# Kernel optimization log

Hardware: AMD Instinct MI355X
Metric: run time of the kernel (lower is better)

## Reference

```python
import jax, jax.numpy as jnp
import numpy as np
from jax import lax

STATE_SIZE = 80
HIDDEN = 512
NC = 1
H = W = 32
STEPS = 64  # steps_range=(64,64)
THRESH = 0.01


def _maxpool3(x):
    # MaxPool2d(3, stride=1, padding=1) on NCHW
    return lax.reduce_window(x, -jnp.inf, lax.max, (1, 1, 3, 3), (1, 1, 1, 1), 'SAME')


def _conv3x3(x, w, b):
    y = lax.conv_general_dilated(x, w, (1, 1), 'SAME',
                                 dimension_numbers=('NCHW', 'OIHW', 'NCHW'))
    return y + b[None, :, None, None]


def _conv1x1(x, w, b):
    # w: (O, I, 1, 1) -> pointwise einsum
    return jnp.einsum('oi,bihw->bohw', w[:, :, 0, 0], x) + b[None, :, None, None]


def setup_inputs() -> dict:
    key = jax.random.key(0)
    ks = jax.random.split(key, 7)
    z = jax.random.normal(ks[0], (8, 100, 1, 1), dtype=jnp.float32)
    W1 = jax.random.normal(ks[1], (HIDDEN, STATE_SIZE, 3, 3), jnp.float32) / np.sqrt(STATE_SIZE * 9)
    b1 = jax.random.normal(ks[2], (HIDDEN,), jnp.float32) * 0.01
    W2 = jax.random.normal(ks[3], (HIDDEN, HIDDEN, 1, 1), jnp.float32) / np.sqrt(HIDDEN)
    b2 = jax.random.normal(ks[4], (HIDDEN,), jnp.float32) * 0.01
    # original code zero-inits the last conv; use small random weights so grads flow
    W3 = jax.random.normal(ks[5], (STATE_SIZE, HIDDEN, 1, 1), jnp.float32) * (0.01 / np.sqrt(HIDDEN))
    b3 = jax.random.normal(ks[6], (STATE_SIZE,), jnp.float32) * 0.001
    return {'z': z, 'W1': W1, 'b1': b1, 'W2': W2, 'b2': b2, 'W3': W3, 'b3': b3}


def _forward(z, W1, b1, W2, b2, W3, b3):
    N = z.shape[0]
    cH, cW = H // 2, W // 2
    state = jnp.zeros((N, STATE_SIZE, H, W), dtype=z.dtype)
    init_hidden = z[:, :STATE_SIZE - 1, 0, 0]  # (N, 79)
    state = state.at[:, 1:, cH, cW].set(init_hidden)
    state = state.at[:, 0, cH, cW].set(1.0)

    keys = jax.random.split(jax.random.key(42), STEPS)

    def ca_step(state, step_key):
        pre_living = _maxpool3(state[:, 0:1]) > THRESH
        perception = _conv3x3(state, W1, b1)
        h = jax.nn.relu(_conv1x1(perception, W2, b2))
        updates = _conv1x1(h, W3, b3)
        # stochastic update with p=1 (rand < 1 is always True, kept for fidelity)
        mask = jax.random.uniform(step_key, (state.shape[0], 1, H, W)) < 1.0
        state = state + mask.astype(state.dtype) * updates
        post_living = _maxpool3(state[:, 0:1]) > THRESH
        living = (post_living & pre_living).astype(state.dtype)
        return state * living, None

    state, _ = lax.scan(ca_step, state, keys)
    return state[:, :NC]  # (N, 1, H, W)


def reference(z, W1, b1, W2, b2, W3, b3):
    return _forward(z, W1, b1, W2, b2, W3, b3)
```

## Files before the change

### kernel.cpp

```cpp
#include <hip/hip_runtime.h>


#define NPIX 8192
#define T_ALIVE 0.01f

typedef _Float16 f16;
typedef __attribute__((ext_vector_type(8)))  _Float16 h8_t;
typedef __attribute__((ext_vector_type(4)))  _Float16 h4_t;
typedef __attribute__((ext_vector_type(16))) float    fx16;

__global__ __launch_bounds__(256) void tr512(
    const float* __restrict__ W2, float* __restrict__ W2T)
{
    __shared__ float t[32][33];
    const int bx = blockIdx.x & 15, by = blockIdx.x >> 4;
    const int x = threadIdx.x & 31, y8 = threadIdx.x >> 5;
#pragma unroll
    for (int r = 0; r < 32; r += 8)
        t[r + y8][x] = W2[(size_t)(by * 32 + r + y8) * 512 + bx * 32 + x];
    __syncthreads();
#pragma unroll
    for (int r = 0; r < 32; r += 8)
        W2T[(size_t)(bx * 32 + r + y8) * 512 + by * 32 + x] = t[x][r + y8];
}

__global__ __launch_bounds__(256) void wc32(
    const float* __restrict__ W2T, const float* __restrict__ W1,
    float* __restrict__ Wc)
{
    __shared__ float As[16][32];
    __shared__ float Bs[16][32];
    const int tid = threadIdx.x;
    const int ty = tid >> 3, tx = tid & 7;
    const int m0 = blockIdx.y * 32, n0 = blockIdx.x * 32;
    float acc[4] = {0.f, 0.f, 0.f, 0.f};

    for (int k0 = 0; k0 < 512; k0 += 16) {
#pragma unroll
        for (int t = 0; t < 2; ++t) {
            const int idx = tid + t * 256;
            const int r = idx >> 5, c = idx & 31;
            As[r][c] = W2T[(size_t)(k0 + r) * 512 + m0 + c];
            const int n = n0 + c;
            Bs[r][c] = (n < 720) ? W1[(size_t)(k0 + r) * 720 + n] : 0.f;
        }
        __syncthreads();
#pragma unroll
        for (int kk = 0; kk < 16; ++kk) {
            const float a = As[kk][ty];
#pragma unroll
            for (int j = 0; j < 4; ++j)
                acc[j] = fmaf(a, Bs[kk][tx * 4 + j], acc[j]);
        }
        __syncthreads();
    }
    const int m = m0 + ty;
#pragma unroll
    for (int j = 0; j < 4; ++j) {
        const int n = n0 + tx * 4 + j;
        if (n < 720) Wc[(size_t)m * 720 + n] = acc[j];
    }
}

__global__ __launch_bounds__(256) void bc_k(
    const float* __restrict__ W2, const float* __restrict__ b1,
    const float* __restrict__ b2, float* __restrict__ bc)
{
    const int m = blockIdx.x * 256 + threadIdx.x;
    if (m >= 512) return;
    float a = b2[m];
    for (int h = 0; h < 512; ++h) a += W2[m * 512 + h] * b1[h];
    bc[m] = a;
}

__global__ __launch_bounds__(256) void swz_wc2(
    const float* __restrict__ Wc, f16* __restrict__ Wcsw2)
{
    const int idx = blockIdx.x * 256 + threadIdx.x;
    if (idx >= 45 * 16 * 64) return;
    const int lane = idx & 63;
    const int t = idx >> 6;
    const int mtg = t & 15, ks = t >> 4;
    const int m = mtg * 32 + (lane & 31);
    const int k0 = ks * 16 + (lane >> 5) * 8;
    h8_t v;
#pragma unroll
    for (int j = 0; j < 8; ++j) {
        const int kp = k0 + j;
        const int tap = kp / 80, ci = kp - tap * 80;
        v[j] = (f16)Wc[(size_t)m * 720 + ci * 9 + tap];
    }
    *(h8_t*)(Wcsw2 + (size_t)idx * 8) = v;
}

__global__ __launch_bounds__(256) void swz_w32(
    const float* __restrict__ W3, f16* __restrict__ W3sw2)
{
    const int idx = blockIdx.x * 256 + threadIdx.x;
    if (idx >= 32 * 3 * 64) return;
    const int lane = idx & 63;
    const int t = idx >> 6;
    const int mt = t % 3, ks2 = t / 3;
    const int m = mt * 32 + (lane & 31);
    const int k0 = ks2 * 16 + (lane >> 5) * 8;
    h8_t v;
#pragma unroll
    for (int j = 0; j < 8; ++j)
        v[j] = (f16)((m < 80) ? W3[(size_t)m * 512 + k0 + j] : 0.f);
    *(h8_t*)(W3sw2 + (size_t)idx * 8) = v;
}

__global__ __launch_bounds__(256) void seed2(
    const float* __restrict__ z, float* __restrict__ U0,
    float* __restrict__ A0)
{
    const int idx = blockIdx.x * 256 + threadIdx.x;
    if (idx >= 640) return;
    const int b = idx / 80, c = idx - b * 80;
    const int n = b * 1024 + 16 * 32 + 16;
    const float v = (c == 0) ? 1.f : z[b * 100 + (c - 1)];
    U0[(size_t)c * NPIX + n] = v;
    if (c == 0) A0[n] = 1.f;
}

__global__ __launch_bounds__(512) void kS(
    const f16* __restrict__ Wcsw2, const float* __restrict__ bc,
    const f16* __restrict__ W3sw2, const float* __restrict__ b3,
    const float* __restrict__ Uin, const float* __restrict__ Ain,
    float* __restrict__ Uout, float* __restrict__ Aout)
{
    __shared__ f16   msT[8160];
    __shared__ f16   Hsw[16384];
    __shared__ float bcL[512];
    __shared__ float b3L[80];
    __shared__ float SrowL[2560];
    __shared__ float N5[160];
    __shared__ float A5[160];
    __shared__ float live3[96];

    const int tid = threadIdx.x;
    const int lane = tid & 63, w = tid >> 6;
    const int li = lane & 31, q2 = lane >> 5;
    const int blk = blockIdx.x;
    const int b = blk >> 5, y = blk & 31;
    const int gb = b * 1024;

    h8_t abuf[8][2];
#pragma unroll
    for (int pk = 0; pk < 8; ++pk)
#pragma unroll
        for (int i = 0; i < 2; ++i)
            abuf[pk][i] = *(const h8_t*)(Wcsw2 +
                (((size_t)pk * 16 + (w * 2 + i)) * 64 + lane) * 8);

    bcL[tid] = bc[tid];
    if (tid < 80) b3L[tid] = b3[tid];

    if (tid < 160) {
        const int r = tid >> 5, x = tid & 31, yy = y - 2 + r;
        const bool ok = ((unsigned)yy < 32u);
        N5[tid] = ok ? Uin[gb + yy * 32 + x] : -1e30f;
        A5[tid] = ok ? Ain[gb + yy * 32 + x] : -1e30f;
    }
    {
        h8_t zz;
#pragma unroll
        for (int j = 0; j < 8; ++j) zz[j] = (f16)0.f;
        for (int i = tid; i < 1020; i += 512)
            *(h8_t*)(msT + (size_t)i * 8) = zz;
    }
    __syncthreads();

    if (tid < 96) {
        const int r = tid >> 5, x = tid & 31;
        float mN = -1e30f, mA = -1e30f;
#pragma unroll
        for (int rr = 0; rr < 3; ++rr)
#pragma unroll
            for (int dx = -1; dx <= 1; ++dx) {
                const int xx = x + dx;
                if ((unsigned)xx < 32u) {
                    mN = fmaxf(mN, N5[(r + rr) * 32 + xx]);
                    mA = fmaxf(mA, A5[(r + rr) * 32 + xx]);
                }
            }
        live3[tid] = (mN > T_ALIVE && mA > T_ALIVE) ? 1.f : 0.f;
    }
    __syncthreads();

#pragma unroll
    for (int it = 0; it < 15; ++it) {
        const int e = tid + it * 512;
        const int x = e & 31;
        const int t2 = e >> 5;
        const int r = t2 / 80, ch = t2 - r * 80;
        const int yy = y - 1 + r;
        float v = 0.f;
        if ((unsigned)yy < 32u)
            v = Uin[(size_t)ch * NPIX + gb + yy * 32 + x] * live3[r * 32 + x];
        msT[(size_t)((ch >> 3) * 102 + r * 34 + x + 1) * 8 + (ch & 7)] = (f16)v;
        if (r == 1) {
            SrowL[ch * 32 + x] = v;
            if (ch == 0) Aout[gb + y * 32 + x] = v;
        }
    }
    __syncthreads();

    int pxh[9];
#pragma unroll
    for (int t = 0; t < 9; ++t)
        pxh[t] = ((t / 3) * 34 + li + (t % 3)) * 8;

    fx16 acc[2];
#pragma unroll
    for (int i = 0; i < 2; ++i)
#pragma unroll
        for (int r = 0; r < 16; ++r) acc[i][r] = 0.f;

#pragma unroll
    for (int ks = 0; ks < 45; ++ks) {
        const int o0 = 2 * ks, o1 = 2 * ks + 1;
        const int a0 = (o0 % 10) * 816 + pxh[o0 / 10];
        const int a1 = (o1 % 10) * 816 + pxh[o1 / 10];
        const h8_t bf = *(const h8_t*)(msT + (q2 ? a1 : a0));
        h8_t av[2];
#pragma unroll
        for (int i = 0; i < 2; ++i) av[i] = abuf[ks & 7][i];
        if (ks + 8 < 45) {
#pragma unroll
            for (int i = 0; i < 2; ++i)
                abuf[ks & 7][i] = *(const h8_t*)(Wcsw2 +
                    (((size_t)(ks + 8) * 16 + (w * 2 + i)) * 64 + lane) * 8);
        }
#pragma unroll
        for (int i = 0; i < 2; ++i)
            acc[i] = __builtin_amdgcn_mfma_f32_32x32x16_f16(
                av[i], bf, acc[i], 0, 0, 0);
    }

#pragma unroll
    for (int i = 0; i < 2; ++i) {
#pragma unroll
        for (int aa = 0; aa < 4; ++aa) {
            const int chl = i * 32 + 8 * aa + 4 * q2;
            const int co = w * 8 + i * 4 + aa;
            h4_t v4;
#pragma unroll
            for (int rb = 0; rb < 4; ++rb)
                v4[rb] = (f16)fmaxf(acc[i][aa * 4 + rb] + bcL[w * 64 + chl + rb], 0.f);
            *(h4_t*)(Hsw + ((size_t)co * 32 + li) * 8 + 4 * q2) = v4;
        }
    }
    __syncthreads();

    if (w < 3) {
        const int mt = w;
        h8_t ar[8];
#pragma unroll
        for (int pk = 0; pk < 8; ++pk)
            ar[pk] = *(const h8_t*)(W3sw2 +
                (((size_t)pk * 3 + mt) * 64 + lane) * 8);

        fx16 acc3;
#pragma unroll
        for (int r = 0; r < 16; ++r) acc3[r] = 0.f;
#pragma unroll
        for (int ks2 = 0; ks2 < 32; ++ks2) {
            const h8_t bf = *(const h8_t*)(Hsw +
                ((size_t)(ks2 * 2 + q2) * 32 + li) * 8);
            const h8_t a = ar[ks2 & 7];
            if (ks2 + 8 < 32)
                ar[ks2 & 7] = *(const h8_t*)(W3sw2 +
                    (((size_t)(ks2 + 8) * 3 + mt) * 64 + lane) * 8);
            acc3 = __builtin_amdgcn_mfma_f32_32x32x16_f16(a, bf, acc3, 0, 0, 0);
        }

        const size_t px = (size_t)(gb + y * 32 + li);
#pragma unroll
        for (int aa = 0; aa < 4; ++aa)
#pragma unroll
            for (int rb = 0; rb < 4; ++rb) {
                const int ch = mt * 32 + rb + 8 * aa + 4 * q2;
                if (ch < 80) {
                    Uout[(size_t)ch * NPIX + px] =
                        SrowL[ch * 32 + li] + acc3[aa * 4 + rb] + b3L[ch];
                }
            }
    }
}

__global__ __launch_bounds__(128) void kF(
    const float* __restrict__ Uf, const float* __restrict__ Af,
    float* __restrict__ dout)
{
    __shared__ float N3[96];
    __shared__ float A3[96];
    const int tid = threadIdx.x;
    const int blk = blockIdx.x;
    const int b = blk >> 5, y = blk & 31;
    const int gb = b * 1024;

    if (tid < 96) {
        const int r = tid >> 5, x = tid & 31, yy = y - 1 + r;
        const bool ok = ((unsigned)yy < 32u);
        N3[tid] = ok ? Uf[gb + yy * 32 + x] : -1e30f;
        A3[tid] = ok ? Af[gb + yy * 32 + x] : -1e30f;
    }
    __syncthreads();

    if (tid < 32) {
        float mN = -1e30f, mA = -1e30f;
#pragma unroll
        for (int rr = 0; rr < 3; ++rr)
#pragma unroll
            for (int dx = -1; dx <= 1; ++dx) {
                const int xx = tid + dx;
                if ((unsigned)xx < 32u) {
                    mN = fmaxf(mN, N3[rr * 32 + xx]);
                    mA = fmaxf(mA, A3[rr * 32 + xx]);
                }
            }
        const float lv = (mN > T_ALIVE && mA > T_ALIVE) ? 1.f : 0.f;
        dout[gb + y * 32 + tid] = Uf[gb + y * 32 + tid] * lv;
    }
}

extern "C" void kernel_launch(void* const* d_in, const int* in_sizes, int n_in,
                              void* d_out, int out_size, void* d_ws, size_t ws_size,
                              hipStream_t stream)
{
    const float* z  = (const float*)d_in[0];
    const float* W1 = (const float*)d_in[1];
    const float* b1 = (const float*)d_in[2];
    const float* W2 = (const float*)d_in[3];
    const float* b2 = (const float*)d_in[4];
    const float* W3 = (const float*)d_in[5];
    const float* b3 = (const float*)d_in[6];

    char* ws = (char*)d_ws;
    float* U0    = (float*)ws;  ws += (size_t)80 * NPIX * 4;
    float* U1    = (float*)ws;  ws += (size_t)80 * NPIX * 4;
    float* A0    = (float*)ws;  ws += (size_t)NPIX * 4;
    float* A1    = (float*)ws;  ws += (size_t)NPIX * 4;
    float* bc    = (float*)ws;  ws += 512 * 4;
    float* Wc    = (float*)ws;  ws += (size_t)512 * 720 * 4;
    float* W2T   = (float*)ws;  ws += (size_t)512 * 512 * 4;
    f16*   Wcsw2 = (f16*)ws;   ws += (size_t)45 * 16 * 64 * 8 * 2;
    f16*   W3sw2 = (f16*)ws;   ws += (size_t)32 * 3 * 64 * 8 * 2;

    hipMemsetAsync(U0, 0, (size_t)80 * NPIX * 4, stream);
    hipMemsetAsync(A0, 0, (size_t)NPIX * 4, stream);
    seed2<<<3, 256, 0, stream>>>(z, U0, A0);
    tr512<<<256, 256, 0, stream>>>(W2, W2T);
    wc32<<<dim3(23, 16), 256, 0, stream>>>(W2T, W1, Wc);
    bc_k<<<2, 256, 0, stream>>>(W2, b1, b2, bc);
    swz_wc2<<<180, 256, 0, stream>>>(Wc, Wcsw2);
    swz_w32<<<24, 256, 0, stream>>>(W3, W3sw2);

    float* Uc = U0;  float* Un = U1;
    float* Ac = A0;  float* An = A1;
    for (int s = 0; s < 64; ++s) {
        kS<<<256, 512, 0, stream>>>(Wcsw2, bc, W3sw2, b3, Uc, Ac, Un, An);
        float* t = Uc; Uc = Un; Un = t;
        float* a = Ac; Ac = An; An = a;
    }
    kF<<<256, 128, 0, stream>>>(Uc, Ac, (float*)d_out);
}
```

Measured before the change: 1.126 ms.

## Process two image rows per block with 1024 threads to reuse weight fragments

```diff
diff --git a/kernel.cpp b/kernel.cpp
--- a/kernel.cpp
+++ b/kernel.cpp
@@ -123,55 +123,55 @@
     if (c == 0) A0[n] = 1.f;
 }
 
-__global__ __launch_bounds__(512) void kS(
+__global__ __launch_bounds__(1024) void kS(
     const f16* __restrict__ Wcsw2, const float* __restrict__ bc,
     const f16* __restrict__ W3sw2, const float* __restrict__ b3,
     const float* __restrict__ Uin, const float* __restrict__ Ain,
     float* __restrict__ Uout, float* __restrict__ Aout)
 {
-    __shared__ f16   msT[8160];
-    __shared__ f16   Hsw[16384];
+    __shared__ f16   msT[10880];
+    __shared__ f16   Hsw[32768];
     __shared__ float bcL[512];
     __shared__ float b3L[80];
-    __shared__ float SrowL[2560];
-    __shared__ float N5[160];
-    __shared__ float A5[160];
-    __shared__ float live3[96];
+    __shared__ float SrowL[2][2560];
+    __shared__ float N6[192];
+    __shared__ float A6[192];
+    __shared__ float live4[128];
 
     const int tid = threadIdx.x;
     const int lane = tid & 63, w = tid >> 6;
     const int li = lane & 31, q2 = lane >> 5;
     const int blk = blockIdx.x;
-    const int b = blk >> 5, y = blk & 31;
+    const int b = blk >> 4, yg = blk & 15;
+    const int y0 = yg * 2;
     const int gb = b * 1024;
 
-    h8_t abuf[8][2];
-#pragma unroll
-    for (int pk = 0; pk < 8; ++pk)
-#pragma unroll
-        for (int i = 0; i < 2; ++i)
-            abuf[pk][i] = *(const h8_t*)(Wcsw2 +
-                (((size_t)pk * 16 + (w * 2 + i)) * 64 + lane) * 8);
-
-    bcL[tid] = bc[tid];
-    if (tid < 80) b3L[tid] = b3[tid];
-
-    if (tid < 160) {
-        const int r = tid >> 5, x = tid & 31, yy = y - 2 + r;
+    h8_t aring[6];
+#pragma unroll
+    for (int pk = 0; pk < 6; ++pk)
+        aring[pk] = *(const h8_t*)(Wcsw2 +
+            (((size_t)pk * 16 + w) * 64 + lane) * 8);
+
+    if (tid < 512) bcL[tid] = bc[tid];
+    if (tid < 80)  b3L[tid] = b3[tid];
+
+    if (tid < 192) {
+        const int r = tid >> 5, x = tid & 31, yy = y0 - 2 + r;
         const bool ok = ((unsigned)yy < 32u);
-        N5[tid] = ok ? Uin[gb + yy * 32 + x] : -1e30f;
-        A5[tid] = ok ? Ain[gb + yy * 32 + x] : -1e30f;
-    }
-    {
+        N6[tid] = ok ? Uin[gb + yy * 32 + x] : -1e30f;
+        A6[tid] = ok ? Ain[gb + yy * 32 + x] : -1e30f;
+    }
+    if (tid < 80) {
+        const int cc = tid >> 3, rem = tid & 7;
+        const int r = rem >> 1, xi = (rem & 1) * 33;
         h8_t zz;
 #pragma unroll
         for (int j = 0; j < 8; ++j) zz[j] = (f16)0.f;
-        for (int i = tid; i < 1020; i += 512)
-            *(h8_t*)(msT + (size_t)i * 8) = zz;
-    }
-    __syncthreads();
-
-    if (tid < 96) {
+        *(h8_t*)(msT + (size_t)(cc * 136 + r * 34 + xi) * 8) = zz;
+    }
+    __syncthreads();
+
+    if (tid < 128) {
         const int r = tid >> 5, x = tid & 31;
         float mN = -1e30f, mA = -1e30f;
 #pragma unroll
@@ -180,28 +180,28 @@
             for (int dx = -1; dx <= 1; ++dx) {
                 const int xx = x + dx;
                 if ((unsigned)xx < 32u) {
-                    mN = fmaxf(mN, N5[(r + rr) * 32 + xx]);
-                    mA = fmaxf(mA, A5[(r + rr) * 32 + xx]);
+                    mN = fmaxf(mN, N6[(r + rr) * 32 + xx]);
+                    mA = fmaxf(mA, A6[(r + rr) * 32 + xx]);
                 }
             }
-        live3[tid] = (mN > T_ALIVE && mA > T_ALIVE) ? 1.f : 0.f;
-    }
-    __syncthreads();
-
-#pragma unroll
-    for (int it = 0; it < 15; ++it) {
-        const int e = tid + it * 512;
+        live4[tid] = (mN > T_ALIVE && mA > T_ALIVE) ? 1.f : 0.f;
+    }
+    __syncthreads();
+
+#pragma unroll
+    for (int it = 0; it < 10; ++it) {
+        const int e = tid + it * 1024;
         const int x = e & 31;
         const int t2 = e >> 5;
         const int r = t2 / 80, ch = t2 - r * 80;
-        const int yy = y - 1 + r;
+        const int yy = y0 - 1 + r;
         float v = 0.f;
         if ((unsigned)yy < 32u)
-            v = Uin[(size_t)ch * NPIX + gb + yy * 32 + x] * live3[r * 32 + x];
-        msT[(size_t)((ch >> 3) * 102 + r * 34 + x + 1) * 8 + (ch & 7)] = (f16)v;
-        if (r == 1) {
-            SrowL[ch * 32 + x] = v;
-            if (ch == 0) Aout[gb + y * 32 + x] = v;
+            v = Uin[(size_t)ch * NPIX + gb + yy * 32 + x] * live4[r * 32 + x];
+        msT[(size_t)((ch >> 3) * 136 + r * 34 + x + 1) * 8 + (ch & 7)] = (f16)v;
+        if (r == 1 || r == 2) {
+            SrowL[r - 1][ch * 32 + x] = v;
+            if (ch == 0) Aout[gb + (y0 + r - 1) * 32 + x] = v;
         }
     }
     __syncthreads();
@@ -211,50 +211,44 @@
     for (int t = 0; t < 9; ++t)
         pxh[t] = ((t / 3) * 34 + li + (t % 3)) * 8;
 
-    fx16 acc[2];
-#pragma unroll
-    for (int i = 0; i < 2; ++i)
-#pragma unroll
-        for (int r = 0; r < 16; ++r) acc[i][r] = 0.f;
+    fx16 acc0, acc1;
+#pragma unroll
+    for (int r = 0; r < 16; ++r) { acc0[r] = 0.f; acc1[r] = 0.f; }
 
 #pragma unroll
     for (int ks = 0; ks < 45; ++ks) {
         const int o0 = 2 * ks, o1 = 2 * ks + 1;
-        const int a0 = (o0 % 10) * 816 + pxh[o0 / 10];
-        const int a1 = (o1 % 10) * 816 + pxh[o1 / 10];
-        const h8_t bf = *(const h8_t*)(msT + (q2 ? a1 : a0));
-        h8_t av[2];
-#pragma unroll
-        for (int i = 0; i < 2; ++i) av[i] = abuf[ks & 7][i];
-        if (ks + 8 < 45) {
-#pragma unroll
-            for (int i = 0; i < 2; ++i)
-                abuf[ks & 7][i] = *(const h8_t*)(Wcsw2 +
-                    (((size_t)(ks + 8) * 16 + (w * 2 + i)) * 64 + lane) * 8);
-        }
-#pragma unroll
-        for (int i = 0; i < 2; ++i)
-            acc[i] = __builtin_amdgcn_mfma_f32_32x32x16_f16(
-                av[i], bf, acc[i], 0, 0, 0);
-    }
-
-#pragma unroll
-    for (int i = 0; i < 2; ++i) {
-#pragma unroll
-        for (int aa = 0; aa < 4; ++aa) {
-            const int chl = i * 32 + 8 * aa + 4 * q2;
-            const int co = w * 8 + i * 4 + aa;
-            h4_t v4;
-#pragma unroll
-            for (int rb = 0; rb < 4; ++rb)
-                v4[rb] = (f16)fmaxf(acc[i][aa * 4 + rb] + bcL[w * 64 + chl + rb], 0.f);
-            *(h4_t*)(Hsw + ((size_t)co * 32 + li) * 8 + 4 * q2) = v4;
-        }
-    }
-    __syncthreads();
-
-    if (w < 3) {
-        const int mt = w;
+        const int a0 = (o0 % 10) * 1088 + pxh[o0 / 10];
+        const int a1 = (o1 % 10) * 1088 + pxh[o1 / 10];
+        const int ab = q2 ? a1 : a0;
+        const h8_t bf0 = *(const h8_t*)(msT + ab);
+        const h8_t bf1 = *(const h8_t*)(msT + ab + 272);
+        const h8_t av = aring[ks % 6];
+        if (ks + 6 < 45)
+            aring[ks % 6] = *(const h8_t*)(Wcsw2 +
+                (((size_t)(ks + 6) * 16 + w) * 64 + lane) * 8);
+        acc0 = __builtin_amdgcn_mfma_f32_32x32x16_f16(av, bf0, acc0, 0, 0, 0);
+        acc1 = __builtin_amdgcn_mfma_f32_32x32x16_f16(av, bf1, acc1, 0, 0, 0);
+    }
+
+#pragma unroll
+    for (int aa = 0; aa < 4; ++aa) {
+        const int chl = 8 * aa + 4 * q2;
+        const int co = w * 4 + aa;
+        h4_t v0, v1;
+#pragma unroll
+        for (int rb = 0; rb < 4; ++rb) {
+            const float bb = bcL[w * 32 + chl + rb];
+            v0[rb] = (f16)fmaxf(acc0[aa * 4 + rb] + bb, 0.f);
+            v1[rb] = (f16)fmaxf(acc1[aa * 4 + rb] + bb, 0.f);
+        }
+        *(h4_t*)(Hsw + ((size_t)co * 64 +      li) * 8 + 4 * q2) = v0;
+        *(h4_t*)(Hsw + ((size_t)co * 64 + 32 + li) * 8 + 4 * q2) = v1;
+    }
+    __syncthreads();
+
+    if (w < 6) {
+        const int mt = w >> 1, r = w & 1;
         h8_t ar[8];
 #pragma unroll
         for (int pk = 0; pk < 8; ++pk)
@@ -263,11 +257,11 @@
 
         fx16 acc3;
 #pragma unroll
-        for (int r = 0; r < 16; ++r) acc3[r] = 0.f;
+        for (int rr = 0; rr < 16; ++rr) acc3[rr] = 0.f;
 #pragma unroll
         for (int ks2 = 0; ks2 < 32; ++ks2) {
             const h8_t bf = *(const h8_t*)(Hsw +
-                ((size_t)(ks2 * 2 + q2) * 32 + li) * 8);
+                ((size_t)(ks2 * 2 + q2) * 64 + r * 32 + li) * 8);
             const h8_t a = ar[ks2 & 7];
             if (ks2 + 8 < 32)
                 ar[ks2 & 7] = *(const h8_t*)(W3sw2 +
@@ -275,7 +269,7 @@
             acc3 = __builtin_amdgcn_mfma_f32_32x32x16_f16(a, bf, acc3, 0, 0, 0);
         }
 
-        const size_t px = (size_t)(gb + y * 32 + li);
+        const size_t px = (size_t)(gb + (y0 + r) * 32 + li);
 #pragma unroll
         for (int aa = 0; aa < 4; ++aa)
 #pragma unroll
@@ -283,7 +277,7 @@
                 const int ch = mt * 32 + rb + 8 * aa + 4 * q2;
                 if (ch < 80) {
                     Uout[(size_t)ch * NPIX + px] =
-                        SrowL[ch * 32 + li] + acc3[aa * 4 + rb] + b3L[ch];
+                        SrowL[r][ch * 32 + li] + acc3[aa * 4 + rb] + b3L[ch];
                 }
             }
     }
@@ -360,7 +354,7 @@
     float* Uc = U0;  float* Un = U1;
     float* Ac = A0;  float* An = A1;
     for (int s = 0; s < 64; ++s) {
-        kS<<<256, 512, 0, stream>>>(Wcsw2, bc, W3sw2, b3, Uc, Ac, Un, An);
+        kS<<<128, 1024, 0, stream>>>(Wcsw2, bc, W3sw2, b3, Uc, Ac, Un, An);
         float* t = Uc; Uc = Un; Un = t;
         float* a = Ac; Ac = An; An = a;
     }
```

Result: slower. 1.294 ms (+15.0%).

## Split CA step into hidden-layer and update kernels with weight-sliced tiling

Applied to the files above, without the earlier changes.

```diff
diff --git a/kernel.cpp b/kernel.cpp
--- a/kernel.cpp
+++ b/kernel.cpp
@@ -8,6 +8,13 @@
 typedef __attribute__((ext_vector_type(8)))  _Float16 h8_t;
 typedef __attribute__((ext_vector_type(4)))  _Float16 h4_t;
 typedef __attribute__((ext_vector_type(16))) float    fx16;
+
+__device__ __forceinline__ void gld16(const f16* g, f16* l)
+{
+    __builtin_amdgcn_global_load_lds(
+        (const __attribute__((address_space(1))) unsigned int*)(const void*)g,
+        (__attribute__((address_space(3))) unsigned int*)(void*)l, 16, 0, 0);
+}
 
 __global__ __launch_bounds__(256) void tr512(
     const float* __restrict__ W2, float* __restrict__ W2T)
@@ -73,24 +80,30 @@
     bc[m] = a;
 }
 
-__global__ __launch_bounds__(256) void swz_wc2(
-    const float* __restrict__ Wc, f16* __restrict__ Wcsw2)
+__global__ __launch_bounds__(256) void swz_wh(
+    const float* __restrict__ Wc, f16* __restrict__ Wh)
 {
     const int idx = blockIdx.x * 256 + threadIdx.x;
-    if (idx >= 45 * 16 * 64) return;
+    if (idx >= 49152) return;
     const int lane = idx & 63;
-    const int t = idx >> 6;
-    const int mtg = t & 15, ks = t >> 4;
+    int t = idx >> 6;
+    const int i = t & 1; t >>= 1;
+    const int ck = t % 48, h = t / 48;
+    const int mtg = h * 2 + i;
     const int m = mtg * 32 + (lane & 31);
-    const int k0 = ks * 16 + (lane >> 5) * 8;
+    const int k0 = ck * 16 + (lane >> 5) * 8;
     h8_t v;
 #pragma unroll
     for (int j = 0; j < 8; ++j) {
         const int kp = k0 + j;
-        const int tap = kp / 80, ci = kp - tap * 80;
-        v[j] = (f16)Wc[(size_t)m * 720 + ci * 9 + tap];
-    }
-    *(h8_t*)(Wcsw2 + (size_t)idx * 8) = v;
+        if (kp < 720) {
+            const int tap = kp / 80, ci = kp - tap * 80;
+            v[j] = (f16)Wc[(size_t)m * 720 + ci * 9 + tap];
+        } else {
+            v[j] = (f16)0.f;
+        }
+    }
+    *(h8_t*)(Wh + (size_t)idx * 8) = v;
 }
 
 __global__ __launch_bounds__(256) void swz_w32(
@@ -110,9 +123,9 @@
     *(h8_t*)(W3sw2 + (size_t)idx * 8) = v;
 }
 
-__global__ __launch_bounds__(256) void seed2(
+__global__ __launch_bounds__(256) void seed3(
     const float* __restrict__ z, float* __restrict__ U0,
-    float* __restrict__ A0)
+    f16* __restrict__ Um0, float* __restrict__ A0)
 {
     const int idx = blockIdx.x * 256 + threadIdx.x;
     if (idx >= 640) return;
@@ -120,23 +133,150 @@
     const int n = b * 1024 + 16 * 32 + 16;
     const float v = (c == 0) ? 1.f : z[b * 100 + (c - 1)];
     U0[(size_t)c * NPIX + n] = v;
+    Um0[(size_t)n * 80 + c] = (f16)v;
     if (c == 0) A0[n] = 1.f;
 }
 
-__global__ __launch_bounds__(512) void kS(
-    const f16* __restrict__ Wcsw2, const float* __restrict__ bc,
+__global__ __launch_bounds__(512) void kBH(
+    const f16* __restrict__ Wh, const float* __restrict__ bc,
+    const f16* __restrict__ Um, const float* __restrict__ Nw,
+    const float* __restrict__ Ap, f16* __restrict__ Hout)
+{
+    __shared__ f16   msT[27200];
+    __shared__ f16   Aring[12288];
+    __shared__ float bcL[64];
+    __shared__ float N12[384];
+    __shared__ float A12[384];
+    __shared__ float live10[320];
+
+    const int tid = threadIdx.x;
+    const int lane = tid & 63, w = tid >> 6;
+    const int li = lane & 31, q2 = lane >> 5;
+    const int blk = blockIdx.x;
+    const int h = blk & 7, g = blk >> 3;
+    const int b = g >> 2, y0 = (g & 3) * 8;
+    const int gb = b * 1024;
+    const f16* Whb = Wh + (size_t)h * 49152;
+
+#pragma unroll
+    for (int c = 0; c < 3; ++c)
+        gld16(Whb + (size_t)c * 4096 + w * 512 + lane * 8,
+              Aring + (size_t)c * 4096 + w * 512);
+
+    if (tid < 64) bcL[tid] = bc[h * 64 + tid];
+
+    if (tid < 384) {
+        const int r = tid >> 5, x = tid & 31, yy = y0 - 2 + r;
+        const bool ok = ((unsigned)yy < 32u);
+        N12[tid] = ok ? Nw[gb + yy * 32 + x] : -1e30f;
+        A12[tid] = ok ? Ap[gb + yy * 32 + x] : -1e30f;
+    }
+    __syncthreads();
+
+    if (tid < 320) {
+        const int r = tid >> 5, x = tid & 31;
+        float mN = -1e30f, mA = -1e30f;
+#pragma unroll
+        for (int rr = 0; rr < 3; ++rr)
+#pragma unroll
+            for (int dx = -1; dx <= 1; ++dx) {
+                const int xx = x + dx;
+                if ((unsigned)xx < 32u) {
+                    mN = fmaxf(mN, N12[(r + rr) * 32 + xx]);
+                    mA = fmaxf(mA, A12[(r + rr) * 32 + xx]);
+                }
+            }
+        live10[tid] = (mN > T_ALIVE && mA > T_ALIVE) ? 1.f : 0.f;
+    }
+    __syncthreads();
+
+    {
+        h8_t zz;
+#pragma unroll
+        for (int j = 0; j < 8; ++j) zz[j] = (f16)0.f;
+        for (int q = tid; q < 3200; q += 512) {
+            const int r = q / 320, rem = q - r * 320;
+            const int cc = rem >> 5, x = rem & 31;
+            const int yy = y0 - 1 + r;
+            h8_t v = zz;
+            if (((unsigned)yy < 32u) && live10[r * 32 + x] != 0.f)
+                v = *(const h8_t*)(Um + (size_t)(gb + yy * 32 + x) * 80 + cc * 8);
+            *(h8_t*)(msT + (size_t)((cc * 10 + r) * 34 + x + 1) * 8) = v;
+        }
+        if (tid < 200) {
+            const int cc = tid / 20, rem = tid % 20;
+            const int r = rem >> 1, xi = (rem & 1) * 33;
+            *(h8_t*)(msT + (size_t)((cc * 10 + r) * 34 + xi) * 8) = zz;
+        }
+    }
+    __syncthreads();
+
+    int pxh[9];
+#pragma unroll
+    for (int t = 0; t < 9; ++t)
+        pxh[t] = ((t / 3) * 34 + li + (t % 3)) * 8;
+
+    fx16 acc0, acc1;
+#pragma unroll
+    for (int r = 0; r < 16; ++r) { acc0[r] = 0.f; acc1[r] = 0.f; }
+
+    const int wbase = w * 272;
+
+    for (int c = 0; c < 12; ++c) {
+        asm volatile("s_waitcnt vmcnt(2)" ::: "memory");
+        __builtin_amdgcn_s_barrier();
+        __builtin_amdgcn_sched_barrier(0);
+        const f16* slot = Aring + (c % 3) * 4096;
+#pragma unroll
+        for (int kk = 0; kk < 4; ++kk) {
+            const int ks = c * 4 + kk;
+            if (ks < 45) {
+                const int o = 2 * ks + q2;
+                const int cc = o % 10, t = o / 10;
+                const h8_t bf = *(const h8_t*)(msT + cc * 2720 + wbase + pxh[t]);
+                const h8_t a0 = *(const h8_t*)(slot + (kk * 2 + 0) * 512 + lane * 8);
+                const h8_t a1 = *(const h8_t*)(slot + (kk * 2 + 1) * 512 + lane * 8);
+                acc0 = __builtin_amdgcn_mfma_f32_32x32x16_f16(a0, bf, acc0, 0, 0, 0);
+                acc1 = __builtin_amdgcn_mfma_f32_32x32x16_f16(a1, bf, acc1, 0, 0, 0);
+            }
+        }
+        __builtin_amdgcn_sched_barrier(0);
+        __builtin_amdgcn_s_barrier();
+        if (c + 3 < 12)
+            gld16(Whb + (size_t)(c + 3) * 4096 + w * 512 + lane * 8,
+                  Aring + (size_t)(c % 3) * 4096 + w * 512);
+    }
+
+    const int R = b * 32 + y0 + w;
+#pragma unroll
+    for (int i = 0; i < 2; ++i) {
+#pragma unroll
+        for (int aa = 0; aa < 4; ++aa) {
+            const int chl = i * 32 + 8 * aa + 4 * q2;
+            const int co = h * 8 + i * 4 + aa;
+            h4_t v4;
+            const fx16& ac = i ? acc1 : acc0;
+#pragma unroll
+            for (int rb = 0; rb < 4; ++rb)
+                v4[rb] = (f16)fmaxf(ac[aa * 4 + rb] + bcL[chl + rb], 0.f);
+            *(h4_t*)(Hout + ((size_t)(R * 64 + co) * 32 + li) * 8 + 4 * q2) = v4;
+        }
+    }
+}
+
+__global__ __launch_bounds__(256) void kU(
     const f16* __restrict__ W3sw2, const float* __restrict__ b3,
-    const float* __restrict__ Uin, const float* __restrict__ Ain,
-    float* __restrict__ Uout, float* __restrict__ Aout)
-{
-    __shared__ f16   msT[8160];
-    __shared__ f16   Hsw[16384];
-    __shared__ float bcL[512];
+    const f16* __restrict__ Hin, const float* __restrict__ Uin,
+    const float* __restrict__ Ain,
+    float* __restrict__ Uout, f16* __restrict__ Umout,
+    float* __restrict__ Aout)
+{
+    __shared__ float SrowL[2560];
+    __shared__ float UrowL[2560];
+    __shared__ float N3[96];
+    __shared__ float A3[96];
+    __shared__ float liveR[32];
     __shared__ float b3L[80];
-    __shared__ float SrowL[2560];
-    __shared__ float N5[160];
-    __shared__ float A5[160];
-    __shared__ float live3[96];
 
     const int tid = threadIdx.x;
     const int lane = tid & 63, w = tid >> 6;
@@ -144,148 +284,89 @@
     const int blk = blockIdx.x;
     const int b = blk >> 5, y = blk & 31;
     const int gb = b * 1024;
-
-    h8_t abuf[8][2];
-#pragma unroll
-    for (int pk = 0; pk < 8; ++pk)
-#pragma unroll
-        for (int i = 0; i < 2; ++i)
-            abuf[pk][i] = *(const h8_t*)(Wcsw2 +
-                (((size_t)pk * 16 + (w * 2 + i)) * 64 + lane) * 8);
-
-    bcL[tid] = bc[tid];
+    const int base = gb + y * 32;
+    const f16* Hrow = Hin + (size_t)blk * 16384;
+
+    h8_t ar[8], hr[8];
+    if (w < 3) {
+#pragma unroll
+        for (int pk = 0; pk < 8; ++pk) {
+            ar[pk] = *(const h8_t*)(W3sw2 + (((size_t)pk * 3 + w) * 64 + lane) * 8);
+            hr[pk] = *(const h8_t*)(Hrow + ((size_t)(pk * 2 + q2) * 32 + li) * 8);
+        }
+    }
     if (tid < 80) b3L[tid] = b3[tid];
-
-    if (tid < 160) {
-        const int r = tid >> 5, x = tid & 31, yy = y - 2 + r;
+    if (tid < 96) {
+        const int r = tid >> 5, x = tid & 31, yy = y - 1 + r;
         const bool ok = ((unsigned)yy < 32u);
-        N5[tid] = ok ? Uin[gb + yy * 32 + x] : -1e30f;
-        A5[tid] = ok ? Ain[gb + yy * 32 + x] : -1e30f;
-    }
-    {
-        h8_t zz;
-#pragma unroll
-        for (int j = 0; j < 8; ++j) zz[j] = (f16)0.f;
-        for (int i = tid; i < 1020; i += 512)
-            *(h8_t*)(msT + (size_t)i * 8) = zz;
-    }
-    __syncthreads();
-
-    if (tid < 96) {
-        const int r = tid >> 5, x = tid & 31;
+        N3[tid] = ok ? Uin[gb + yy * 32 + x] : -1e30f;
+        A3[tid] = ok ? Ain[gb + yy * 32 + x] : -1e30f;
+    }
+    __syncthreads();
+
+    if (tid < 32) {
         float mN = -1e30f, mA = -1e30f;
 #pragma unroll
         for (int rr = 0; rr < 3; ++rr)
 #pragma unroll
             for (int dx = -1; dx <= 1; ++dx) {
-                const int xx = x + dx;
+                const int xx = tid + dx;
                 if ((unsigned)xx < 32u) {
-                    mN = fmaxf(mN, N5[(r + rr) * 32 + xx]);
-                    mA = fmaxf(mA, A5[(r + rr) * 32 + xx]);
+                    mN = fmaxf(mN, N3[rr * 32 + xx]);
+                    mA = fmaxf(mA, A3[rr * 32 + xx]);
                 }
             }
-        live3[tid] = (mN > T_ALIVE && mA > T_ALIVE) ? 1.f : 0.f;
-    }
-    __syncthreads();
-
-#pragma unroll
-    for (int it = 0; it < 15; ++it) {
-        const int e = tid + it * 512;
-        const int x = e & 31;
-        const int t2 = e >> 5;
-        const int r = t2 / 80, ch = t2 - r * 80;
-        const int yy = y - 1 + r;
-        float v = 0.f;
-        if ((unsigned)yy < 32u)
-            v = Uin[(size_t)ch * NPIX + gb + yy * 32 + x] * live3[r * 32 + x];
-        msT[(size_t)((ch >> 3) * 102 + r * 34 + x + 1) * 8 + (ch & 7)] = (f16)v;
-        if (r == 1) {
-            SrowL[ch * 32 + x] = v;
-            if (ch == 0) Aout[gb + y * 32 + x] = v;
-        }
-    }
-    __syncthreads();
-
-    int pxh[9];
-#pragma unroll
-    for (int t = 0; t < 9; ++t)
-        pxh[t] = ((t / 3) * 34 + li + (t % 3)) * 8;
-
-    fx16 acc[2];
-#pragma unroll
-    for (int i = 0; i < 2; ++i)
-#pragma unroll
-        for (int r = 0; r < 16; ++r) acc[i][r] = 0.f;
-
-#pragma unroll
-    for (int ks = 0; ks < 45; ++ks) {
-        const int o0 = 2 * ks, o1 = 2 * ks + 1;
-        const int a0 = (o0 % 10) * 816 + pxh[o0 / 10];
-        const int a1 = (o1 % 10) * 816 + pxh[o1 / 10];
-        const h8_t bf = *(const h8_t*)(msT + (q2 ? a1 : a0));
-        h8_t av[2];
-#pragma unroll
-        for (int i = 0; i < 2; ++i) av[i] = abuf[ks & 7][i];
-        if (ks + 8 < 45) {
-#pragma unroll
-            for (int i = 0; i < 2; ++i)
-                abuf[ks & 7][i] = *(const h8_t*)(Wcsw2 +
-                    (((size_t)(ks + 8) * 16 + (w * 2 + i)) * 64 + lane) * 8);
-        }
-#pragma unroll
-        for (int i = 0; i < 2; ++i)
-            acc[i] = __builtin_amdgcn_mfma_f32_32x32x16_f16(
-                av[i], bf, acc[i], 0, 0, 0);
-    }
-
-#pragma unroll
-    for (int i = 0; i < 2; ++i) {
-#pragma unroll
-        for (int aa = 0; aa < 4; ++aa) {
-            const int chl = i * 32 + 8 * aa + 4 * q2;
-            const int co = w * 8 + i * 4 + aa;
-            h4_t v4;
-#pragma unroll
-            for (int rb = 0; rb < 4; ++rb)
-                v4[rb] = (f16)fmaxf(acc[i][aa * 4 + rb] + bcL[w * 64 + chl + rb], 0.f);
-            *(h4_t*)(Hsw + ((size_t)co * 32 + li) * 8 + 4 * q2) = v4;
-        }
+        liveR[tid] = (mN > T_ALIVE && mA > T_ALIVE) ? 1.f : 0.f;
+    }
+    __syncthreads();
+
+#pragma unroll
+    for (int it = 0; it < 10; ++it) {
+        const int q = tid + it * 256;
+        const int ch = q >> 5, x = q & 31;
+        const float v = Uin[(size_t)ch * NPIX + base + x] * liveR[x];
+        SrowL[q] = v;
+        if (ch == 0) Aout[base + x] = v;
     }
     __syncthreads();
 
     if (w < 3) {
-        const int mt = w;
-        h8_t ar[8];
-#pragma unroll
-        for (int pk = 0; pk < 8; ++pk)
-            ar[pk] = *(const h8_t*)(W3sw2 +
-                (((size_t)pk * 3 + mt) * 64 + lane) * 8);
-
         fx16 acc3;
 #pragma unroll
         for (int r = 0; r < 16; ++r) acc3[r] = 0.f;
 #pragma unroll
         for (int ks2 = 0; ks2 < 32; ++ks2) {
-            const h8_t bf = *(const h8_t*)(Hsw +
-                ((size_t)(ks2 * 2 + q2) * 32 + li) * 8);
             const h8_t a = ar[ks2 & 7];
-            if (ks2 + 8 < 32)
+            const h8_t bf = hr[ks2 & 7];
+            if (ks2 + 8 < 32) {
                 ar[ks2 & 7] = *(const h8_t*)(W3sw2 +
-                    (((size_t)(ks2 + 8) * 3 + mt) * 64 + lane) * 8);
+                    (((size_t)(ks2 + 8) * 3 + w) * 64 + lane) * 8);
+                hr[ks2 & 7] = *(const h8_t*)(Hrow +
+                    ((size_t)((ks2 + 8) * 2 + q2) * 32 + li) * 8);
+            }
             acc3 = __builtin_amdgcn_mfma_f32_32x32x16_f16(a, bf, acc3, 0, 0, 0);
         }
-
-        const size_t px = (size_t)(gb + y * 32 + li);
 #pragma unroll
         for (int aa = 0; aa < 4; ++aa)
 #pragma unroll
             for (int rb = 0; rb < 4; ++rb) {
-                const int ch = mt * 32 + rb + 8 * aa + 4 * q2;
+                const int ch = w * 32 + rb + 8 * aa + 4 * q2;
                 if (ch < 80) {
-                    Uout[(size_t)ch * NPIX + px] =
-                        SrowL[ch * 32 + li] + acc3[aa * 4 + rb] + b3L[ch];
+                    const float uv = SrowL[ch * 32 + li] + acc3[aa * 4 + rb] + b3L[ch];
+                    Uout[(size_t)ch * NPIX + base + li] = uv;
+                    UrowL[ch * 32 + li] = uv;
                 }
             }
+    }
+    __syncthreads();
+
+    for (int q = tid; q < 640; q += 256) {
+        const int cq = q >> 5, x = q & 31;
+        h4_t v4;
+#pragma unroll
+        for (int rb = 0; rb < 4; ++rb)
+            v4[rb] = (f16)UrowL[(cq * 4 + rb) * 32 + x];
+        *(h4_t*)(Umout + (size_t)(base + x) * 80 + cq * 4) = v4;
     }
 }
 
@@ -340,28 +421,35 @@
     char* ws = (char*)d_ws;
     float* U0    = (float*)ws;  ws += (size_t)80 * NPIX * 4;
     float* U1    = (float*)ws;  ws += (size_t)80 * NPIX * 4;
+    f16*   Um0   = (f16*)ws;   ws += (size_t)NPIX * 80 * 2;
+    f16*   Um1   = (f16*)ws;   ws += (size_t)NPIX * 80 * 2;
     float* A0    = (float*)ws;  ws += (size_t)NPIX * 4;
     float* A1    = (float*)ws;  ws += (size_t)NPIX * 4;
+    f16*   Hbuf  = (f16*)ws;   ws += (size_t)256 * 64 * 32 * 8 * 2;
     float* bc    = (float*)ws;  ws += 512 * 4;
     float* Wc    = (float*)ws;  ws += (size_t)512 * 720 * 4;
     float* W2T   = (float*)ws;  ws += (size_t)512 * 512 * 4;
-    f16*   Wcsw2 = (f16*)ws;   ws += (size_t)45 * 16 * 64 * 8 * 2;
+    f16*   Wh    = (f16*)ws;   ws += (size_t)49152 * 8 * 2;
     f16*   W3sw2 = (f16*)ws;   ws += (size_t)32 * 3 * 64 * 8 * 2;
 
     hipMemsetAsync(U0, 0, (size_t)80 * NPIX * 4, stream);
+    hipMemsetAsync(Um0, 0, (size_t)NPIX * 80 * 2, stream);
     hipMemsetAsync(A0, 0, (size_t)NPIX * 4, stream);
-    seed2<<<3, 256, 0, stream>>>(z, U0, A0);
+    seed3<<<3, 256, 0, stream>>>(z, U0, Um0, A0);
     tr512<<<256, 256, 0, stream>>>(W2, W2T);
     wc32<<<dim3(23, 16), 256, 0, stream>>>(W2T, W1, Wc);
     bc_k<<<2, 256, 0, stream>>>(W2, b1, b2, bc);
-    swz_wc2<<<180, 256, 0, stream>>>(Wc, Wcsw2);
+    swz_wh<<<192, 256, 0, stream>>>(Wc, Wh);
     swz_w32<<<24, 256, 0, stream>>>(W3, W3sw2);
 
     float* Uc = U0;  float* Un = U1;
+    f16*   Mc = Um0; f16*   Mn = Um1;
     float* Ac = A0;  float* An = A1;
     for (int s = 0; s < 64; ++s) {
-        kS<<<256, 512, 0, stream>>>(Wcsw2, bc, W3sw2, b3, Uc, Ac, Un, An);
+        kBH<<<256, 512, 0, stream>>>(Wh, bc, Mc, Uc, Ac, Hbuf);
+        kU<<<256, 256, 0, stream>>>(W3sw2, b3, Hbuf, Uc, Ac, Un, Mn, An);
         float* t = Uc; Uc = Un; Un = t;
+        f16*   m = Mc; Mc = Mn; Mn = m;
         float* a = Ac; Ac = An; An = a;
     }
     kF<<<256, 128, 0, stream>>>(Uc, Ac, (float*)d_out);
```

Result: slower. 1.450 ms (+28.8%).

## Split-K the fused step kernel across 16 waves with LDS partial-sum reduction

Applied to the files above, without the earlier changes.

```diff
diff --git a/kernel.cpp b/kernel.cpp
--- a/kernel.cpp
+++ b/kernel.cpp
@@ -123,7 +123,7 @@
     if (c == 0) A0[n] = 1.f;
 }
 
-__global__ __launch_bounds__(512) void kS(
+__global__ __launch_bounds__(1024) void kS(
     const f16* __restrict__ Wcsw2, const float* __restrict__ bc,
     const f16* __restrict__ W3sw2, const float* __restrict__ b3,
     const float* __restrict__ Uin, const float* __restrict__ Ain,
@@ -131,9 +131,9 @@
 {
     __shared__ f16   msT[8160];
     __shared__ f16   Hsw[16384];
+    __shared__ float Pacc[16384];
     __shared__ float bcL[512];
     __shared__ float b3L[80];
-    __shared__ float SrowL[2560];
     __shared__ float N5[160];
     __shared__ float A5[160];
     __shared__ float live3[96];
@@ -141,20 +141,23 @@
     const int tid = threadIdx.x;
     const int lane = tid & 63, w = tid >> 6;
     const int li = lane & 31, q2 = lane >> 5;
+    const int mg = w & 7, kh = w >> 3;
     const int blk = blockIdx.x;
     const int b = blk >> 5, y = blk & 31;
     const int gb = b * 1024;
 
-    h8_t abuf[8][2];
-#pragma unroll
-    for (int pk = 0; pk < 8; ++pk)
-#pragma unroll
-        for (int i = 0; i < 2; ++i)
-            abuf[pk][i] = *(const h8_t*)(Wcsw2 +
-                (((size_t)pk * 16 + (w * 2 + i)) * 64 + lane) * 8);
-
-    bcL[tid] = bc[tid];
-    if (tid < 80) b3L[tid] = b3[tid];
+    const f16* abase = Wcsw2 + ((size_t)(mg * 2) * 64 + lane) * 8;
+    const int KB0 = kh ? 23 : 0;
+    h8_t ring0[6], ring1[6];
+#pragma unroll
+    for (int pk = 0; pk < 6; ++pk) {
+        const f16* p = abase + (size_t)(KB0 + pk) * 8192;
+        ring0[pk] = *(const h8_t*)(p);
+        ring1[pk] = *(const h8_t*)(p + 512);
+    }
+
+    if (tid < 512) bcL[tid] = bc[tid];
+    if (tid < 80)  b3L[tid] = b3[tid];
 
     if (tid < 160) {
         const int r = tid >> 5, x = tid & 31, yy = y - 2 + r;
@@ -162,12 +165,13 @@
         N5[tid] = ok ? Uin[gb + yy * 32 + x] : -1e30f;
         A5[tid] = ok ? Ain[gb + yy * 32 + x] : -1e30f;
     }
-    {
+    if (tid < 60) {
+        const int cc = tid / 6, rem = tid % 6;
+        const int r = rem >> 1, xi = (rem & 1) * 33;
         h8_t zz;
 #pragma unroll
         for (int j = 0; j < 8; ++j) zz[j] = (f16)0.f;
-        for (int i = tid; i < 1020; i += 512)
-            *(h8_t*)(msT + (size_t)i * 8) = zz;
+        *(h8_t*)(msT + (size_t)(cc * 102 + r * 34 + xi) * 8) = zz;
     }
     __syncthreads();
 
@@ -188,21 +192,16 @@
     }
     __syncthreads();
 
-#pragma unroll
-    for (int it = 0; it < 15; ++it) {
-        const int e = tid + it * 512;
-        const int x = e & 31;
-        const int t2 = e >> 5;
+    for (int q = tid; q < 7680; q += 1024) {
+        const int x = q & 31;
+        const int t2 = q >> 5;
         const int r = t2 / 80, ch = t2 - r * 80;
         const int yy = y - 1 + r;
         float v = 0.f;
         if ((unsigned)yy < 32u)
             v = Uin[(size_t)ch * NPIX + gb + yy * 32 + x] * live3[r * 32 + x];
         msT[(size_t)((ch >> 3) * 102 + r * 34 + x + 1) * 8 + (ch & 7)] = (f16)v;
-        if (r == 1) {
-            SrowL[ch * 32 + x] = v;
-            if (ch == 0) Aout[gb + y * 32 + x] = v;
-        }
+        if (r == 1 && ch == 0) Aout[gb + y * 32 + x] = v;
     }
     __syncthreads();
 
@@ -211,79 +210,136 @@
     for (int t = 0; t < 9; ++t)
         pxh[t] = ((t / 3) * 34 + li + (t % 3)) * 8;
 
-    fx16 acc[2];
-#pragma unroll
-    for (int i = 0; i < 2; ++i)
-#pragma unroll
-        for (int r = 0; r < 16; ++r) acc[i][r] = 0.f;
-
-#pragma unroll
-    for (int ks = 0; ks < 45; ++ks) {
-        const int o0 = 2 * ks, o1 = 2 * ks + 1;
-        const int a0 = (o0 % 10) * 816 + pxh[o0 / 10];
-        const int a1 = (o1 % 10) * 816 + pxh[o1 / 10];
-        const h8_t bf = *(const h8_t*)(msT + (q2 ? a1 : a0));
-        h8_t av[2];
-#pragma unroll
-        for (int i = 0; i < 2; ++i) av[i] = abuf[ks & 7][i];
-        if (ks + 8 < 45) {
-#pragma unroll
-            for (int i = 0; i < 2; ++i)
-                abuf[ks & 7][i] = *(const h8_t*)(Wcsw2 +
-                    (((size_t)(ks + 8) * 16 + (w * 2 + i)) * 64 + lane) * 8);
-        }
-#pragma unroll
-        for (int i = 0; i < 2; ++i)
-            acc[i] = __builtin_amdgcn_mfma_f32_32x32x16_f16(
-                av[i], bf, acc[i], 0, 0, 0);
-    }
-
-#pragma unroll
-    for (int i = 0; i < 2; ++i) {
-#pragma unroll
-        for (int aa = 0; aa < 4; ++aa) {
-            const int chl = i * 32 + 8 * aa + 4 * q2;
-            const int co = w * 8 + i * 4 + aa;
-            h4_t v4;
-#pragma unroll
-            for (int rb = 0; rb < 4; ++rb)
-                v4[rb] = (f16)fmaxf(acc[i][aa * 4 + rb] + bcL[w * 64 + chl + rb], 0.f);
-            *(h4_t*)(Hsw + ((size_t)co * 32 + li) * 8 + 4 * q2) = v4;
-        }
-    }
-    __syncthreads();
-
-    if (w < 3) {
-        const int mt = w;
+    fx16 acc0, acc1;
+#pragma unroll
+    for (int r = 0; r < 16; ++r) { acc0[r] = 0.f; acc1[r] = 0.f; }
+
+    if (kh == 0) {
+#pragma unroll
+        for (int kk = 0; kk < 23; ++kk) {
+            const int ks = kk;
+            const int o0 = 2 * ks, o1 = 2 * ks + 1;
+            const int a0 = (o0 % 10) * 816 + pxh[o0 / 10];
+            const int a1 = (o1 % 10) * 816 + pxh[o1 / 10];
+            const h8_t bf = *(const h8_t*)(msT + (q2 ? a1 : a0));
+            const h8_t av0 = ring0[kk % 6], av1 = ring1[kk % 6];
+            if (kk + 6 < 23) {
+                const f16* p = abase + (size_t)(ks + 6) * 8192;
+                ring0[kk % 6] = *(const h8_t*)(p);
+                ring1[kk % 6] = *(const h8_t*)(p + 512);
+            }
+            acc0 = __builtin_amdgcn_mfma_f32_32x32x16_f16(av0, bf, acc0, 0, 0, 0);
+            acc1 = __builtin_amdgcn_mfma_f32_32x32x16_f16(av1, bf, acc1, 0, 0, 0);
+        }
+    } else {
+#pragma unroll
+        for (int kk = 0; kk < 22; ++kk) {
+            const int ks = 23 + kk;
+            const int o0 = 2 * ks, o1 = 2 * ks + 1;
+            const int a0 = (o0 % 10) * 816 + pxh[o0 / 10];
+            const int a1 = (o1 % 10) * 816 + pxh[o1 / 10];
+            const h8_t bf = *(const h8_t*)(msT + (q2 ? a1 : a0));
+            const h8_t av0 = ring0[kk % 6], av1 = ring1[kk % 6];
+            if (kk + 6 < 22) {
+                const f16* p = abase + (size_t)(ks + 6) * 8192;
+                ring0[kk % 6] = *(const h8_t*)(p);
+                ring1[kk % 6] = *(const h8_t*)(p + 512);
+            }
+            acc0 = __builtin_amdgcn_mfma_f32_32x32x16_f16(av0, bf, acc0, 0, 0, 0);
+            acc1 = __builtin_amdgcn_mfma_f32_32x32x16_f16(av1, bf, acc1, 0, 0, 0);
+        }
+    }
+
+    if (kh == 1) {
+#pragma unroll
+        for (int r = 0; r < 16; ++r) {
+            Pacc[((size_t)(mg * 2 + 0) * 16 + r) * 64 + lane] = acc0[r];
+            Pacc[((size_t)(mg * 2 + 1) * 16 + r) * 64 + lane] = acc1[r];
+        }
+    }
+    __syncthreads();
+    if (kh == 0) {
+#pragma unroll
+        for (int r = 0; r < 16; ++r) {
+            acc0[r] += Pacc[((size_t)(mg * 2 + 0) * 16 + r) * 64 + lane];
+            acc1[r] += Pacc[((size_t)(mg * 2 + 1) * 16 + r) * 64 + lane];
+        }
+#pragma unroll
+        for (int i = 0; i < 2; ++i) {
+#pragma unroll
+            for (int aa = 0; aa < 4; ++aa) {
+                const int chl = i * 32 + 8 * aa + 4 * q2;
+                const int co = mg * 8 + i * 4 + aa;
+                h4_t v4;
+                const fx16& ac = i ? acc1 : acc0;
+#pragma unroll
+                for (int rb = 0; rb < 4; ++rb)
+                    v4[rb] = (f16)fmaxf(ac[aa * 4 + rb] + bcL[mg * 64 + chl + rb], 0.f);
+                *(h4_t*)(Hsw + ((size_t)co * 32 + li) * 8 + 4 * q2) = v4;
+            }
+        }
+    }
+    __syncthreads();
+
+    fx16 acc3;
+#pragma unroll
+    for (int r = 0; r < 16; ++r) acc3[r] = 0.f;
+    const bool p2a = (w < 3);
+    const bool p2b = (w >= 8 && w < 11);
+    if (p2a || p2b) {
+        const int mt = mg;
+        const int kb = p2b ? 16 : 0;
         h8_t ar[8];
 #pragma unroll
         for (int pk = 0; pk < 8; ++pk)
             ar[pk] = *(const h8_t*)(W3sw2 +
-                (((size_t)pk * 3 + mt) * 64 + lane) * 8);
-
-        fx16 acc3;
-#pragma unroll
-        for (int r = 0; r < 16; ++r) acc3[r] = 0.f;
-#pragma unroll
-        for (int ks2 = 0; ks2 < 32; ++ks2) {
-            const h8_t bf = *(const h8_t*)(Hsw +
-                ((size_t)(ks2 * 2 + q2) * 32 + li) * 8);
-            const h8_t a = ar[ks2 & 7];
-            if (ks2 + 8 < 32)
-                ar[ks2 & 7] = *(const h8_t*)(W3sw2 +
-                    (((size_t)(ks2 + 8) * 3 + mt) * 64 + lane) * 8);
-            acc3 = __builtin_amdgcn_mfma_f32_32x32x16_f16(a, bf, acc3, 0, 0, 0);
-        }
+                (((size_t)(kb + pk) * 3 + mt) * 64 + lane) * 8);
+        if (p2a) {
+#pragma unroll
+            for (int i = 0; i < 16; ++i) {
+                const h8_t bfh = *(const h8_t*)(Hsw +
+                    ((size_t)(i * 2 + q2) * 32 + li) * 8);
+                const h8_t a = ar[i & 7];
+                if (i + 8 < 16)
+                    ar[i & 7] = *(const h8_t*)(W3sw2 +
+                        (((size_t)(i + 8) * 3 + mt) * 64 + lane) * 8);
+                acc3 = __builtin_amdgcn_mfma_f32_32x32x16_f16(a, bfh, acc3, 0, 0, 0);
+            }
+        } else {
+#pragma unroll
+            for (int i = 0; i < 16; ++i) {
+                const int ks2 = 16 + i;
+                const h8_t bfh = *(const h8_t*)(Hsw +
+                    ((size_t)(ks2 * 2 + q2) * 32 + li) * 8);
+                const h8_t a = ar[i & 7];
+                if (i + 8 < 16)
+                    ar[i & 7] = *(const h8_t*)(W3sw2 +
+                        (((size_t)(ks2 + 8) * 3 + mt) * 64 + lane) * 8);
+                acc3 = __builtin_amdgcn_mfma_f32_32x32x16_f16(a, bfh, acc3, 0, 0, 0);
+            }
+        }
+    }
+    if (p2b) {
+#pragma unroll
+        for (int r = 0; r < 16; ++r)
+            Pacc[((size_t)mg * 16 + r) * 64 + lane] = acc3[r];
+    }
+    __syncthreads();
+    if (p2a) {
+#pragma unroll
+        for (int r = 0; r < 16; ++r)
+            acc3[r] += Pacc[((size_t)w * 16 + r) * 64 + lane];
 
         const size_t px = (size_t)(gb + y * 32 + li);
+        const float lv = live3[32 + li];
 #pragma unroll
         for (int aa = 0; aa < 4; ++aa)
 #pragma unroll
             for (int rb = 0; rb < 4; ++rb) {
-                const int ch = mt * 32 + rb + 8 * aa + 4 * q2;
+                const int ch = w * 32 + rb + 8 * aa + 4 * q2;
                 if (ch < 80) {
-                    Uout[(size_t)ch * NPIX + px] =
-                        SrowL[ch * 32 + li] + acc3[aa * 4 + rb] + b3L[ch];
+                    const size_t idx = (size_t)ch * NPIX + px;
+                    Uout[idx] = Uin[idx] * lv + acc3[aa * 4 + rb] + b3L[ch];
                 }
             }
     }
@@ -360,7 +416,7 @@
     float* Uc = U0;  float* Un = U1;
     float* Ac = A0;  float* An = A1;
     for (int s = 0; s < 64; ++s) {
-        kS<<<256, 512, 0, stream>>>(Wcsw2, bc, W3sw2, b3, Uc, Ac, Un, An);
+        kS<<<256, 1024, 0, stream>>>(Wcsw2, bc, W3sw2, b3, Uc, Ac, Un, An);
         float* t = Uc; Uc = Un; Un = t;
         float* a = Ac; Ac = An; An = a;
     }
```

New measurement: 1.207 ms. 7.2% more time.
